# Performance work log

Measured on AMD Instinct MI355X. Metric: run time of the kernel, lower is better.

Reference implementation:

```python
import jax, jax.numpy as jnp
import numpy as np

VOXEL_SIZE = 96
SHARPNESS = 100.0
EPS = 1e-8


def _grid_coords(V):
    # matches torch: x fastest, normalized by (V-1); shape [V*V, 2] as (x, y)
    y, x = jnp.meshgrid(jnp.arange(V, dtype=jnp.float32), jnp.arange(V, dtype=jnp.float32), indexing='ij')
    return jnp.stack([x.ravel(), y.ravel()], axis=1) / float(V - 1)


def setup_inputs() -> dict:
    key = jax.random.key(0)
    k1, k2, k3 = jax.random.split(key, 3)
    B, N, P = 4, 32, 32
    polygons = jax.random.uniform(k1, (B, N, P, 2), dtype=jnp.float32)
    attributes = jax.random.uniform(k2, (B, 8), dtype=jnp.float32)
    validity_scores = jax.random.uniform(k3, (B, N), dtype=jnp.float32)
    return {"polygons": polygons, "attributes": attributes, "validity_scores": validity_scores}


def _polygon_masks(polygons, coords):
    # polygons: [B,N,P,2], coords: [M,2] -> soft occupancy masks [B,N,M]
    v0 = polygons                              # [B,N,P,2]
    v1 = jnp.roll(polygons, -1, axis=2)        # next vertex (closed loop)
    e = v1 - v0                                # edges [B,N,P,2]
    pts = coords[None, None, None]             # [1,1,1,M,2]
    v = pts - v0[:, :, :, None, :]             # [B,N,P,M,2]
    e_sq = (e * e).sum(-1) + EPS               # [B,N,P]
    t = (v * e[:, :, :, None, :]).sum(-1) / e_sq[..., None]   # [B,N,P,M]
    t = jnp.clip(t, 0.0, 1.0)
    proj = v0[:, :, :, None, :] + t[..., None] * e[:, :, :, None, :]
    diff = pts - proj
    dists = jnp.sqrt((diff * diff).sum(-1))    # [B,N,P,M]
    min_dist = dists.min(axis=2)               # [B,N,M] min over edges
    # ray-casting point-in-polygon (horizontal ray toward +x)
    x_pts = coords[:, 0]                        # [M]
    y_pts = coords[:, 1]
    x0, y0 = v0[..., 0:1], v0[..., 1:2]        # [B,N,P,1]
    x1, y1 = v1[..., 0:1], v1[..., 1:2]
    y_crosses = ((y0 <= y_pts) & (y1 > y_pts)) | ((y1 <= y_pts) & (y0 > y_pts))
    inter_x = x0 + (x1 - x0) * ((y_pts - y0) / (y1 - y0 + EPS))
    crossings = (inter_x > x_pts) & y_crosses  # [B,N,P,M]
    inside = (crossings.sum(axis=2) % 2) == 1  # [B,N,M]
    sdf = jnp.where(inside, -min_dist, min_dist)
    return jax.nn.sigmoid(-sdf * SHARPNESS)    # [B,N,M]


def reference(polygons, attributes, validity_scores):
    B = polygons.shape[0]
    V = VOXEL_SIZE
    coords = _grid_coords(V)                                   # [V*V, 2]
    masks = _polygon_masks(polygons, coords)                   # [B,N,M]
    valid = validity_scores >= 0.5                             # [B,N]
    combined = jnp.max(jnp.where(valid[:, :, None], masks, 0.0), axis=1)  # [B,M]
    combined = combined.reshape(B, V, V)                       # [B,H,W]
    # height extrusion: int(round(clamp(attr,0,1)*D)), clamped to [1,D]; non-differentiable
    norm_h = jnp.clip(attributes[:, 0], 0.0, 1.0)
    hv = jnp.clip(jnp.round(norm_h * V), 1.0, float(V))        # [B]
    hv = jax.lax.stop_gradient(hv)
    depth_mask = (jnp.arange(V, dtype=jnp.float32)[None, :] < hv[:, None]).astype(combined.dtype)  # [B,D]
    voxels = combined[:, None, :, :] * depth_mask[:, :, None, None]  # [B,D,H,W]
    return voxels
```

## Files before the change

kernel.cpp:

```cpp
#include <hip/hip_runtime.h>

#define V 96
#define VV (V * V)
#define B_ 4
#define N_ 32
#define P_ 32
#define TPB 512
#define PXB 64
#define TILES_PER_B (VV / PXB)
#define WAVES (TPB / 64)
#define NPW (N_ / WAVES)
#define DPW (V / WAVES)

__global__ __launch_bounds__(TPB) void fused_kernel(
    const float* __restrict__ poly,
    const float* __restrict__ attr,
    const float* __restrict__ validity,
    float* __restrict__ out)
{
    const int b    = blockIdx.x / TILES_PER_B;
    const int tile = blockIdx.x % TILES_PER_B;
    const int t    = threadIdx.x;
    const int wave = t >> 6;
    const int lane = t & 63;

    __shared__ float4 sE[N_][P_][2];
    __shared__ unsigned int red[PXB];

    if (t < PXB) red[t] = 0u;

    for (int k = t; k < N_ * P_; k += TPB) {
        const int n = k >> 5, p = k & 31, pn = (p + 1) & 31;
        const float* base = poly + (size_t)(b * N_ + n) * (P_ * 2);
        float x0 = base[p * 2],  y0 = base[p * 2 + 1];
        float x1 = base[pn * 2], y1 = base[pn * 2 + 1];
        float ex = x1 - x0, ey = y1 - y0;
        float srq = __builtin_amdgcn_rcpf(ex * ex + ey * ey + 1e-8f);
        float sry = __builtin_amdgcn_rcpf(ey + 1e-8f);
        float sI  = ex * sry;
        float cI  = fmaf(-sI, y0, x0);
        sE[n][p][0] = make_float4(x0, y0, ex, ey);
        sE[n][p][1] = make_float4(srq, y1, cI, sI);
    }
    __syncthreads();

    const int pix  = tile * PXB + lane;
    const int py_i = pix / V, px_i = pix - py_i * V;
    const float px = (float)px_i / 95.0f;
    const float py = (float)py_i / 95.0f;

    float best = 0.0f;
    #pragma unroll
    for (int i = 0; i < NPW; ++i) {
        const int n = wave * NPW + i;
        if (validity[b * N_ + n] < 0.5f) continue;

        float mind2 = 1e30f;
        int   par   = 0;
        #pragma unroll
        for (int p = 0; p < P_; ++p) {
            const float4 e0 = sE[n][p][0];
            const float4 e1 = sE[n][p][1];

            float vx = px - e0.x, vy = py - e0.y;
            float tt = (vx * e0.z + vy * e0.w) * e1.x;
            tt = fminf(fmaxf(tt, 0.0f), 1.0f);
            float dx = fmaf(-tt, e0.z, vx), dy = fmaf(-tt, e0.w, vy);
            mind2 = fminf(mind2, fmaf(dx, dx, dy * dy));

            bool c0 = (e0.y <= py);
            bool c1 = (e1.y <= py);
            float ix = fmaf(e1.w, py, e1.z);
            par ^= (int)((c0 != c1) & (ix > px));
        }
        float mind = sqrtf(mind2);
        float sdf  = par ? -mind : mind;
        float m = __builtin_amdgcn_rcpf(
            1.0f + __builtin_amdgcn_exp2f(sdf * 144.26950408889634f));
        best = fmaxf(best, m);
    }
    atomicMax(&red[lane], __float_as_uint(best));
    __syncthreads();

    const float a  = attr[b * 8];
    const float nh = fminf(fmaxf(a, 0.0f), 1.0f);
    const float hv = fminf(fmaxf(rintf(nh * (float)V), 1.0f), (float)V);
    const float c  = __uint_as_float(red[lane]);
    float* obase = out + (size_t)b * V * VV + tile * PXB + lane;
    #pragma unroll
    for (int i = 0; i < DPW; ++i) {
        const int d = wave * DPW + i;
        const float keep = ((float)d < hv) ? 1.0f : 0.0f;
        obase[(size_t)d * VV] = c * keep;
    }
}

extern "C" void kernel_launch(void* const* d_in, const int* in_sizes, int n_in,
                              void* d_out, int out_size, void* d_ws, size_t ws_size,
                              hipStream_t stream) {
    const float* polygons = (const float*)d_in[0];
    const float* attrs    = (const float*)d_in[1];
    const float* validity = (const float*)d_in[2];
    float* out = (float*)d_out;

    fused_kernel<<<B_ * TILES_PER_B, TPB, 0, stream>>>(polygons, attrs, validity, out);
}
```

Baseline: 74.54 us.

## Map lanes to polygon×4-pixel groups to reuse edge loads and go branch-free

Work is remapped so each wave covers four polygons at once, with 16 lanes per polygon and four consecutive pixels per lane. Each edge load and the per-edge row terms (vy·e_y/|e|², the crossing test, and the intercept) are then reused across those four pixels. The per-polygon validity branch becomes a multiply by a 0/1 mask, with an early exit when a whole wave is invalid. Partial maxima are combined with xor-shuffles before the shared atomicMax. The edge array stride is padded to avoid LDS bank conflicts; in exchange, registers per thread go up and invalid polygons are now computed rather than skipped.

```diff
diff --git a/kernel.cpp b/kernel.cpp
--- a/kernel.cpp
+++ b/kernel.cpp
@@ -6,11 +6,10 @@
 #define N_ 32
 #define P_ 32
 #define TPB 512
-#define PXB 64
-#define TILES_PER_B (VV / PXB)
-#define WAVES (TPB / 64)
-#define NPW (N_ / WAVES)
-#define DPW (V / WAVES)
+#define TILE 64
+#define TILES_PER_B (VV / TILE)
+#define PXL 4
+#define ESTRIDE (P_ * 2 + 1)
 
 __global__ __launch_bounds__(TPB) void fused_kernel(
     const float* __restrict__ poly,
@@ -23,11 +22,13 @@
     const int t    = threadIdx.x;
     const int wave = t >> 6;
     const int lane = t & 63;
+    const int psub = lane >> 4;
+    const int xsub = lane & 15;
 
-    __shared__ float4 sE[N_][P_][2];
-    __shared__ unsigned int red[PXB];
+    __shared__ float4 sE[N_ * ESTRIDE];
+    __shared__ float  red[TILE];
 
-    if (t < PXB) red[t] = 0u;
+    if (t < TILE) red[t] = 0.0f;
 
     for (int k = t; k < N_ * P_; k += TPB) {
         const int n = k >> 5, p = k & 31, pn = (p + 1) & 31;
@@ -37,61 +38,75 @@
         float ex = x1 - x0, ey = y1 - y0;
         float srq = __builtin_amdgcn_rcpf(ex * ex + ey * ey + 1e-8f);
         float sry = __builtin_amdgcn_rcpf(ey + 1e-8f);
-        float sI  = ex * sry;
-        float cI  = fmaf(-sI, y0, x0);
-        sE[n][p][0] = make_float4(x0, y0, ex, ey);
-        sE[n][p][1] = make_float4(srq, y1, cI, sI);
+        sE[n * ESTRIDE + p * 2]     = make_float4(x0, y0, ex, ey);
+        sE[n * ESTRIDE + p * 2 + 1] = make_float4(ex * srq, ey * srq, y1, ex * sry);
     }
     __syncthreads();
 
-    const int pix  = tile * PXB + lane;
-    const int py_i = pix / V, px_i = pix - py_i * V;
-    const float px = (float)px_i / 95.0f;
-    const float py = (float)py_i / 95.0f;
+    const int n  = wave * PXL + psub;
+    const float vf = (validity[b * N_ + n] >= 0.5f) ? 1.0f : 0.0f;
 
-    float best = 0.0f;
-    #pragma unroll
-    for (int i = 0; i < NPW; ++i) {
-        const int n = wave * NPW + i;
-        if (validity[b * N_ + n] < 0.5f) continue;
+    if (__ballot(vf != 0.0f) != 0ull) {
+        const int pixb = tile * TILE + xsub * PXL;
+        const int row  = pixb / V;
+        const int col0 = pixb - row * V;
+        const float py = (float)row / 95.0f;
+        float pxv[PXL];
+        #pragma unroll
+        for (int i = 0; i < PXL; ++i) pxv[i] = (float)(col0 + i) / 95.0f;
 
-        float mind2 = 1e30f;
-        int   par   = 0;
+        float mind2[PXL] = {1e30f, 1e30f, 1e30f, 1e30f};
+        int   par[PXL]   = {0, 0, 0, 0};
+
         #pragma unroll
         for (int p = 0; p < P_; ++p) {
-            const float4 e0 = sE[n][p][0];
-            const float4 e1 = sE[n][p][1];
+            const float4 e0 = sE[n * ESTRIDE + p * 2];
+            const float4 e1 = sE[n * ESTRIDE + p * 2 + 1];
 
-            float vx = px - e0.x, vy = py - e0.y;
-            float tt = (vx * e0.z + vy * e0.w) * e1.x;
-            tt = fminf(fmaxf(tt, 0.0f), 1.0f);
-            float dx = fmaf(-tt, e0.z, vx), dy = fmaf(-tt, e0.w, vy);
-            mind2 = fminf(mind2, fmaf(dx, dx, dy * dy));
+            float vy = py - e0.y;
+            float tb = vy * e1.y;
+            float cI = fmaf(-e1.w, e0.y, e0.x);
+            float ix = fmaf(e1.w, py, cI);
+            bool  c0 = (e0.y <= py);
+            bool  c1 = (e1.z <= py);
+            int cross = (int)(c0 != c1);
 
-            bool c0 = (e0.y <= py);
-            bool c1 = (e1.y <= py);
-            float ix = fmaf(e1.w, py, e1.z);
-            par ^= (int)((c0 != c1) & (ix > px));
+            #pragma unroll
+            for (int i = 0; i < PXL; ++i) {
+                float vx = pxv[i] - e0.x;
+                float tt = fmaf(vx, e1.x, tb);
+                tt = fminf(fmaxf(tt, 0.0f), 1.0f);
+                float dx = fmaf(-tt, e0.z, vx);
+                float dy = fmaf(-tt, e0.w, vy);
+                mind2[i] = fminf(mind2[i], fmaf(dx, dx, dy * dy));
+                par[i]  ^= (ix > pxv[i]) ? cross : 0;
+            }
         }
-        float mind = sqrtf(mind2);
-        float sdf  = par ? -mind : mind;
-        float m = __builtin_amdgcn_rcpf(
-            1.0f + __builtin_amdgcn_exp2f(sdf * 144.26950408889634f));
-        best = fmaxf(best, m);
+
+        #pragma unroll
+        for (int i = 0; i < PXL; ++i) {
+            float mind = sqrtf(mind2[i]);
+            float sdf  = par[i] ? -mind : mind;
+            float m = __builtin_amdgcn_rcpf(
+                1.0f + __builtin_amdgcn_exp2f(sdf * 144.26950408889634f));
+            float bst = m * vf;
+            bst = fmaxf(bst, __shfl_xor(bst, 16));
+            bst = fmaxf(bst, __shfl_xor(bst, 32));
+            if (psub == 0)
+                atomicMax((unsigned int*)&red[xsub * PXL + i], __float_as_uint(bst));
+        }
     }
-    atomicMax(&red[lane], __float_as_uint(best));
     __syncthreads();
 
     const float a  = attr[b * 8];
     const float nh = fminf(fmaxf(a, 0.0f), 1.0f);
     const float hv = fminf(fmaxf(rintf(nh * (float)V), 1.0f), (float)V);
-    const float c  = __uint_as_float(red[lane]);
-    float* obase = out + (size_t)b * V * VV + tile * PXB + lane;
+    const float c  = red[lane];
+    float* obase = out + (size_t)b * V * VV + tile * TILE + lane;
     #pragma unroll
-    for (int i = 0; i < DPW; ++i) {
-        const int d = wave * DPW + i;
-        const float keep = ((float)d < hv) ? 1.0f : 0.0f;
-        obase[(size_t)d * VV] = c * keep;
+    for (int i = 0; i < V / 8; ++i) {
+        const int d = wave * (V / 8) + i;
+        obase[(size_t)d * VV] = ((float)d < hv) ? c : 0.0f;
     }
 }
 
```

Result: slower. 83.47 us (+12.0%).
